# Optimization experiments

Measured on AMD Instinct MI355X. Metric: run time of the kernel, lower is better.

Reference implementation:

```python
import jax, jax.numpy as jnp
import numpy as np

MODEL_DIM = 1024
NUM_HEADS = 16
HEAD_DIM = MODEL_DIM // NUM_HEADS


def setup_inputs() -> dict:
    key = jax.random.key(0)
    ks = jax.random.split(key, 9)
    s = 1.0 / np.sqrt(MODEL_DIM)
    d = {
        "query": jax.random.normal(ks[0], (2, 2048, MODEL_DIM), dtype=jnp.float32),
        "Wq": jax.random.normal(ks[1], (MODEL_DIM, MODEL_DIM), dtype=jnp.float32) * s,
        "bq": jnp.zeros((MODEL_DIM,), dtype=jnp.float32),
        "Wk": jax.random.normal(ks[2], (MODEL_DIM, MODEL_DIM), dtype=jnp.float32) * s,
        "bk": jnp.zeros((MODEL_DIM,), dtype=jnp.float32),
        "Wv": jax.random.normal(ks[3], (MODEL_DIM, MODEL_DIM), dtype=jnp.float32) * s,
        "bv": jnp.zeros((MODEL_DIM,), dtype=jnp.float32),
        "Wo": jax.random.normal(ks[4], (MODEL_DIM, MODEL_DIM), dtype=jnp.float32) * s,
        "bo": jnp.zeros((MODEL_DIM,), dtype=jnp.float32),
    }
    return d


def reference(query, Wq, bq, Wk, bk, Wv, bv, Wo, bo):
    B, S, D = query.shape
    H, hd = NUM_HEADS, HEAD_DIM
    # self-attention: key = value = query
    q = (query @ Wq.T + bq).reshape(B, S, H, hd).transpose(0, 2, 1, 3)  # [B,H,S,hd]
    k = (query @ Wk.T + bk).reshape(B, S, H, hd).transpose(0, 2, 1, 3)
    v = (query @ Wv.T + bv).reshape(B, S, H, hd).transpose(0, 2, 1, 3)
    scores = jnp.einsum("bhqd,bhkd->bhqk", q, k) / np.sqrt(hd)  # [B,H,S,S]
    attn = jax.nn.softmax(scores, axis=-1)
    ctx = jnp.einsum("bhqk,bhkd->bhqd", attn, v)  # [B,H,S,hd]
    ctx = ctx.transpose(0, 2, 1, 3).reshape(B, S, D)
    return ctx @ Wo.T + bo
```

## Files before the change

kernel.cpp:

```cpp
#include <hip/hip_runtime.h>

typedef __attribute__((ext_vector_type(8))) __bf16 bf16x8;
typedef __attribute__((ext_vector_type(8))) unsigned short ushort8;
typedef __attribute__((ext_vector_type(4))) unsigned short ushort4v;
typedef __attribute__((ext_vector_type(4))) float f32x4;
typedef __attribute__((ext_vector_type(2))) _Float16 f16x2;
typedef __attribute__((ext_vector_type(4))) _Float16 f16x4;
typedef __attribute__((ext_vector_type(8))) _Float16 f16x8;
typedef __attribute__((ext_vector_type(2))) __fp16 fp16v2;

__device__ __forceinline__ unsigned short f2bf(float f) {
    union { float f; unsigned int u; } c; c.f = f;
    unsigned int u = c.u;
    u += 0x7fffu + ((u >> 16) & 1u);
    return (unsigned short)(u >> 16);
}

__device__ __forceinline__ void async16(const void* g, void* l) {
    __builtin_amdgcn_global_load_lds(
        (const __attribute__((address_space(1))) unsigned int*)g,
        (__attribute__((address_space(3))) unsigned int*)l, 16, 0, 0);
}

__global__ __launch_bounds__(256) void cvt_all(
    const float* __restrict__ q,  const float* __restrict__ wq,
    const float* __restrict__ wk, const float* __restrict__ wv,
    const float* __restrict__ wo,
    unsigned short* __restrict__ q_bf, unsigned short* __restrict__ wqkv,
    unsigned short* __restrict__ wo_bf, float scale_k)
{
    const int NQ = 4096 * 1024, NW = 1024 * 1024;
    int i = (blockIdx.x * 256 + threadIdx.x) * 4;
    const float* src; unsigned short* dst; float sc = 1.0f; int off;
    if (i < NQ)               { src = q;  dst = q_bf;          off = i; }
    else if (i < NQ + NW)     { src = wq; dst = wqkv;          off = i - NQ; }
    else if (i < NQ + 2 * NW) { src = wk; dst = wqkv + NW;     off = i - NQ - NW; sc = scale_k; }
    else if (i < NQ + 3 * NW) { src = wv; dst = wqkv + 2 * NW; off = i - NQ - 2 * NW; }
    else                      { src = wo; dst = wo_bf;         off = i - NQ - 3 * NW; }
    float4 v = *(const float4*)(src + off);
    ushort4v o;
    o[0] = f2bf(v.x * sc); o[1] = f2bf(v.y * sc);
    o[2] = f2bf(v.z * sc); o[3] = f2bf(v.w * sc);
    *(ushort4v*)(dst + off) = o;
}

__global__ __launch_bounds__(256) void qkv_gemm(
    const unsigned short* __restrict__ A,
    const unsigned short* __restrict__ B,
    unsigned short* __restrict__ qkv,
    _Float16* __restrict__ vtg,
    const float* __restrict__ b0, const float* __restrict__ b1, const float* __restrict__ b2,
    float s1)
{
    __shared__ __align__(16) unsigned short As[128 * 64];
    __shared__ __align__(16) unsigned short Bs[128 * 64];

    const int tid  = threadIdx.x;
    const int lane = tid & 63, wave = tid >> 6;
    const int quad = lane >> 4, l15 = lane & 15;
    const int wm = wave >> 1, wn = wave & 1;
    const int by = blockIdx.y, bx = blockIdx.x;
    const int K = 1024;

    const int srow = lane >> 3;
    const int sp   = lane & 7;
    const int scl  = sp ^ srow;
    const int sw   = l15 & 7;

    f32x4 acc[4][4];
#pragma unroll
    for (int i = 0; i < 4; ++i)
#pragma unroll
        for (int j = 0; j < 4; ++j) acc[i][j] = (f32x4)(0.0f);

    for (int kt = 0; kt < 16; ++kt) {
        __syncthreads();
#pragma unroll
        for (int j = 0; j < 4; ++j) {
            int r0 = wave * 32 + j * 8;
            async16(A + (size_t)(by * 128 + r0 + srow) * K + kt * 64 + scl * 8, &As[r0 * 64]);
            async16(B + (size_t)(bx * 128 + r0 + srow) * K + kt * 64 + scl * 8, &Bs[r0 * 64]);
        }
        __syncthreads();

#pragma unroll
        for (int kh = 0; kh < 2; ++kh) {
            bf16x8 af[4], bfr[4];
#pragma unroll
            for (int mi = 0; mi < 4; ++mi)
                af[mi] = __builtin_bit_cast(bf16x8,
                    *(const ushort8*)&As[(wm * 64 + mi * 16 + l15) * 64 + ((kh * 4 + quad) ^ sw) * 8]);
#pragma unroll
            for (int ni = 0; ni < 4; ++ni)
                bfr[ni] = __builtin_bit_cast(bf16x8,
                    *(const ushort8*)&Bs[(wn * 64 + ni * 16 + l15) * 64 + ((kh * 4 + quad) ^ sw) * 8]);
#pragma unroll
            for (int mi = 0; mi < 4; ++mi)
#pragma unroll
                for (int ni = 0; ni < 4; ++ni)
                    acc[mi][ni] = __builtin_amdgcn_mfma_f32_16x16x32_bf16(af[mi], bfr[ni], acc[mi][ni], 0, 0, 0);
        }
    }

    if (bx < 16) {
#pragma unroll
        for (int ni = 0; ni < 4; ++ni) {
            int n = bx * 128 + wn * 64 + ni * 16 + l15;
            float bias = (n < 1024) ? b0[n] : b1[n - 1024] * s1;
#pragma unroll
            for (int mi = 0; mi < 4; ++mi) {
#pragma unroll
                for (int r = 0; r < 4; ++r) {
                    int m = by * 128 + wm * 64 + mi * 16 + quad * 4 + r;
                    qkv[(size_t)m * 2048 + n] = f2bf(acc[mi][ni][r] + bias);
                }
            }
        }
    } else {
        const int mb = by * 128 + wm * 64;
        const int b  = mb >> 11;
        const int st = (mb & 2047) >> 6;
#pragma unroll
        for (int ni = 0; ni < 4; ++ni) {
            int vf = (bx - 16) * 128 + wn * 64 + ni * 16 + l15;
            int h = vf >> 6, hd = vf & 63;
            float bias = b2[vf];
            _Float16* vrow = vtg + ((size_t)((b * 16 + h) * 64 + hd)) * 2048 + st * 64;
#pragma unroll
            for (int mi = 0; mi < 4; ++mi) {
                int p = ((mi >> 1) * 4 + quad) ^ (l15 & 7);
                f16x4 o;
#pragma unroll
                for (int r = 0; r < 4; ++r) o[r] = (_Float16)(acc[mi][ni][r] + bias);
                *(f16x4*)(vrow + p * 8 + (mi & 1) * 4) = o;
            }
        }
    }
}

__global__ __launch_bounds__(256) void out_gemm(
    const unsigned short* __restrict__ A,
    const unsigned short* __restrict__ B,
    float* __restrict__ Cout,
    const float* __restrict__ bo)
{
    __shared__ __align__(16) unsigned short As[128 * 64];
    __shared__ __align__(16) unsigned short Bs[64 * 64];

    const int tid  = threadIdx.x;
    const int lane = tid & 63, wave = tid >> 6;
    const int quad = lane >> 4, l15 = lane & 15;
    const int wm = wave >> 1, wn = wave & 1;
    const int by = blockIdx.y, bx = blockIdx.x;
    const int K = 1024;

    const int srow = lane >> 3;
    const int sp   = lane & 7;
    const int scl  = sp ^ srow;
    const int sw   = l15 & 7;

    f32x4 acc[4][2];
#pragma unroll
    for (int i = 0; i < 4; ++i)
#pragma unroll
        for (int j = 0; j < 2; ++j) acc[i][j] = (f32x4)(0.0f);

    for (int kt = 0; kt < 16; ++kt) {
        __syncthreads();
#pragma unroll
        for (int j = 0; j < 4; ++j) {
            int r0 = wave * 32 + j * 8;
            async16(A + (size_t)(by * 128 + r0 + srow) * K + kt * 64 + scl * 8, &As[r0 * 64]);
        }
#pragma unroll
        for (int j = 0; j < 2; ++j) {
            int r0 = wave * 16 + j * 8;
            async16(B + (size_t)(bx * 64 + r0 + srow) * K + kt * 64 + scl * 8, &Bs[r0 * 64]);
        }
        __syncthreads();

#pragma unroll
        for (int kh = 0; kh < 2; ++kh) {
            bf16x8 af[4], bfr[2];
#pragma unroll
            for (int mi = 0; mi < 4; ++mi)
                af[mi] = __builtin_bit_cast(bf16x8,
                    *(const ushort8*)&As[(wm * 64 + mi * 16 + l15) * 64 + ((kh * 4 + quad) ^ sw) * 8]);
#pragma unroll
            for (int ni = 0; ni < 2; ++ni)
                bfr[ni] = __builtin_bit_cast(bf16x8,
                    *(const ushort8*)&Bs[(wn * 32 + ni * 16 + l15) * 64 + ((kh * 4 + quad) ^ sw) * 8]);
#pragma unroll
            for (int mi = 0; mi < 4; ++mi)
#pragma unroll
                for (int ni = 0; ni < 2; ++ni)
                    acc[mi][ni] = __builtin_amdgcn_mfma_f32_16x16x32_bf16(af[mi], bfr[ni], acc[mi][ni], 0, 0, 0);
        }
    }

#pragma unroll
    for (int ni = 0; ni < 2; ++ni) {
        int n = bx * 64 + wn * 32 + ni * 16 + l15;
        float bias = bo[n];
#pragma unroll
        for (int mi = 0; mi < 4; ++mi) {
#pragma unroll
            for (int r = 0; r < 4; ++r) {
                int m = by * 128 + wm * 64 + mi * 16 + quad * 4 + r;
                Cout[(size_t)m * 1024 + n] = acc[mi][ni][r] + bias;
            }
        }
    }
}

__global__ __launch_bounds__(256) void attn(const unsigned short* __restrict__ qkv,
                                            const _Float16* __restrict__ vtg,
                                            unsigned short* __restrict__ ctx)
{
    __shared__ __align__(16) unsigned short Ks[4 * 64 * 64];
    __shared__ __align__(16) _Float16 Vt[4 * 64 * 64];

    const int tid  = threadIdx.x;
    const int lane = tid & 63, wave = tid >> 6;
    const int quad = lane >> 4, l15 = lane & 15;
    const int bh = blockIdx.y;
    const int b = bh >> 4, h = bh & 15;
    const int q0 = blockIdx.x * 128;

    const int srow = lane >> 3;
    const int sp   = lane & 7;
    const int scl  = sp ^ srow;
    const int sw   = l15 & 7;

    bf16x8 qf[2][2];
#pragma unroll
    for (int s = 0; s < 2; ++s) {
        int qrow = b * 2048 + q0 + wave * 32 + s * 16 + l15;
#pragma unroll
        for (int kh = 0; kh < 2; ++kh)
            qf[s][kh] = __builtin_bit_cast(bf16x8,
                *(const ushort8*)(qkv + (size_t)qrow * 2048 + h * 64 + kh * 32 + quad * 8));
    }

    f32x4 ot[2][4];
#pragma unroll
    for (int s = 0; s < 2; ++s)
#pragma unroll
        for (int ht = 0; ht < 4; ++ht) ot[s][ht] = (f32x4)(0.0f);
    float l_acc[2] = {0.0f, 0.0f};
    const fp16v2 ones = {(__fp16)1.0f, (__fp16)1.0f};

    for (int KT = 0; KT < 8; ++KT) {
        __syncthreads();
#pragma unroll
        for (int j = 0; j < 4; ++j) {
            int kt = KT * 4 + j;
#pragma unroll
            for (int i = 0; i < 2; ++i) {
                int row = i * 32 + wave * 8 + srow;
                async16(qkv + (size_t)(b * 2048 + kt * 64 + row) * 2048 + 1024 + h * 64 + scl * 8,
                        &Ks[j * 4096 + (i * 32 + wave * 8) * 64]);
                async16(vtg + (size_t)(bh * 64 + row) * 2048 + kt * 64 + sp * 8,
                        (unsigned short*)&Vt[j * 4096 + (i * 32 + wave * 8) * 64]);
            }
        }
        __syncthreads();

#pragma unroll
        for (int j = 0; j < 4; ++j) {
            const unsigned short* KsJ = &Ks[j * 4096];
            const _Float16*       VtJ = &Vt[j * 4096];

            f16x4 pv[2][4];
#pragma unroll
            for (int mt = 0; mt < 4; ++mt) {
                const unsigned short* kb = &KsJ[(mt * 16 + l15) * 64];
                bf16x8 k0 = __builtin_bit_cast(bf16x8, *(const ushort8*)(kb + (quad ^ sw) * 8));
                bf16x8 k1 = __builtin_bit_cast(bf16x8, *(const ushort8*)(kb + ((quad ^ sw) ^ 4) * 8));
#pragma unroll
                for (int s = 0; s < 2; ++s) {
                    f32x4 s4 = (f32x4)(0.0f);
                    s4 = __builtin_amdgcn_mfma_f32_16x16x32_bf16(k0, qf[s][0], s4, 0, 0, 0);
                    s4 = __builtin_amdgcn_mfma_f32_16x16x32_bf16(k1, qf[s][1], s4, 0, 0, 0);
                    float p0 = __builtin_amdgcn_exp2f(s4[0]);
                    float p1 = __builtin_amdgcn_exp2f(s4[1]);
                    float p2 = __builtin_amdgcn_exp2f(s4[2]);
                    float p3 = __builtin_amdgcn_exp2f(s4[3]);
                    fp16v2 lo = __builtin_amdgcn_cvt_pkrtz(p0, p1);
                    fp16v2 hi = __builtin_amdgcn_cvt_pkrtz(p2, p3);
                    l_acc[s] = __builtin_amdgcn_fdot2(lo, ones, l_acc[s], false);
                    l_acc[s] = __builtin_amdgcn_fdot2(hi, ones, l_acc[s], false);
                    f16x2 lo2 = __builtin_bit_cast(f16x2, lo);
                    f16x2 hi2 = __builtin_bit_cast(f16x2, hi);
                    pv[s][mt] = __builtin_shufflevector(lo2, hi2, 0, 1, 2, 3);
                }
            }

#pragma unroll
            for (int ht = 0; ht < 4; ++ht) {
                const _Float16* vb = &VtJ[(ht * 16 + l15) * 64];
#pragma unroll
                for (int g = 0; g < 2; ++g) {
                    f16x8 v8 = *(const f16x8*)(vb + (((g * 4 + quad) ^ sw)) * 8);
#pragma unroll
                    for (int s = 0; s < 2; ++s) {
                        f16x8 p8 = __builtin_shufflevector(pv[s][2 * g], pv[s][2 * g + 1],
                                                           0, 1, 2, 3, 4, 5, 6, 7);
                        ot[s][ht] = __builtin_amdgcn_mfma_f32_16x16x32_f16(v8, p8, ot[s][ht], 0, 0, 0);
                    }
                }
            }
        }
    }

#pragma unroll
    for (int s = 0; s < 2; ++s) {
        float l = l_acc[s];
        l += __shfl_xor(l, 16, 64);
        l += __shfl_xor(l, 32, 64);
        float inv = 1.0f / l;
        int qrow = b * 2048 + q0 + wave * 32 + s * 16 + l15;
#pragma unroll
        for (int ht = 0; ht < 4; ++ht) {
            ushort4v o4;
#pragma unroll
            for (int r = 0; r < 4; ++r) o4[r] = f2bf(ot[s][ht][r] * inv);
            *(ushort4v*)(ctx + (size_t)qrow * 1024 + h * 64 + ht * 16 + quad * 4) = o4;
        }
    }
}

extern "C" void kernel_launch(void* const* d_in, const int* in_sizes, int n_in,
                              void* d_out, int out_size, void* d_ws, size_t ws_size,
                              hipStream_t stream) {
    const float* query = (const float*)d_in[0];
    const float* Wq = (const float*)d_in[1];
    const float* bq = (const float*)d_in[2];
    const float* Wk = (const float*)d_in[3];
    const float* bk = (const float*)d_in[4];
    const float* Wv = (const float*)d_in[5];
    const float* bv = (const float*)d_in[6];
    const float* Wo = (const float*)d_in[7];
    const float* bo = (const float*)d_in[8];

    char* ws = (char*)d_ws;
    unsigned short* q_bf  = (unsigned short*)(ws);
    unsigned short* ctx   = (unsigned short*)(ws);
    unsigned short* wqkv  = (unsigned short*)(ws + 8388608);
    unsigned short* wo_bf = (unsigned short*)(ws + 14680064);
    unsigned short* qkv   = (unsigned short*)(ws + 16777216);
    _Float16*       vtg   = (_Float16*)(ws + 33554432);

    const float SCALE = 0.125f * 1.4426950408889634f;

    cvt_all<<<8192, 256, 0, stream>>>(query, Wq, Wk, Wv, Wo, q_bf, wqkv, wo_bf, SCALE);
    qkv_gemm<<<dim3(24, 32), 256, 0, stream>>>(q_bf, wqkv, qkv, vtg, bq, bk, bv, SCALE);
    attn<<<dim3(16, 32), 256, 0, stream>>>(qkv, vtg, ctx);
    out_gemm<<<dim3(16, 32), 256, 0, stream>>>(ctx, wo_bf, (float*)d_out, bo);
}
```

Before: 196.7 us.

## Fuse fp32-to-fp16 conversion into GEMM tile loads and drop the conversion kernel

Removes the separate cvt_all pass and has the QKV and output GEMMs load fp32 inputs and weights directly. Each tile is converted to fp16 in registers with packed round-toward-zero conversion before being written to shared memory. The GEMMs switch from bf16 to fp16 MFMA, and the context buffer becomes fp16. This eliminates one launch and a full bf16 write and re-read of the activations and weights. In exchange, each GEMM block re-reads fp32 data (twice the bytes) through synchronous register loads instead of async global-to-LDS copies, which may expose memory latency. fp16 range and RTZ rounding also change numerics.

```diff
diff --git a/kernel.cpp b/kernel.cpp
--- a/kernel.cpp
+++ b/kernel.cpp
@@ -22,31 +22,24 @@
         (__attribute__((address_space(3))) unsigned int*)l, 16, 0, 0);
 }
 
-__global__ __launch_bounds__(256) void cvt_all(
-    const float* __restrict__ q,  const float* __restrict__ wq,
-    const float* __restrict__ wk, const float* __restrict__ wv,
-    const float* __restrict__ wo,
-    unsigned short* __restrict__ q_bf, unsigned short* __restrict__ wqkv,
-    unsigned short* __restrict__ wo_bf, float scale_k)
-{
-    const int NQ = 4096 * 1024, NW = 1024 * 1024;
-    int i = (blockIdx.x * 256 + threadIdx.x) * 4;
-    const float* src; unsigned short* dst; float sc = 1.0f; int off;
-    if (i < NQ)               { src = q;  dst = q_bf;          off = i; }
-    else if (i < NQ + NW)     { src = wq; dst = wqkv;          off = i - NQ; }
-    else if (i < NQ + 2 * NW) { src = wk; dst = wqkv + NW;     off = i - NQ - NW; sc = scale_k; }
-    else if (i < NQ + 3 * NW) { src = wv; dst = wqkv + 2 * NW; off = i - NQ - 2 * NW; }
-    else                      { src = wo; dst = wo_bf;         off = i - NQ - 3 * NW; }
-    float4 v = *(const float4*)(src + off);
-    ushort4v o;
-    o[0] = f2bf(v.x * sc); o[1] = f2bf(v.y * sc);
-    o[2] = f2bf(v.z * sc); o[3] = f2bf(v.w * sc);
-    *(ushort4v*)(dst + off) = o;
+__device__ __forceinline__ ushort8 cvt8(float4 a, float4 b, float sc) {
+    fp16v2 c0 = __builtin_amdgcn_cvt_pkrtz(a.x * sc, a.y * sc);
+    fp16v2 c1 = __builtin_amdgcn_cvt_pkrtz(a.z * sc, a.w * sc);
+    fp16v2 c2 = __builtin_amdgcn_cvt_pkrtz(b.x * sc, b.y * sc);
+    fp16v2 c3 = __builtin_amdgcn_cvt_pkrtz(b.z * sc, b.w * sc);
+    f16x2 d0 = __builtin_bit_cast(f16x2, c0);
+    f16x2 d1 = __builtin_bit_cast(f16x2, c1);
+    f16x2 d2 = __builtin_bit_cast(f16x2, c2);
+    f16x2 d3 = __builtin_bit_cast(f16x2, c3);
+    f16x4 lo = __builtin_shufflevector(d0, d1, 0, 1, 2, 3);
+    f16x4 hi = __builtin_shufflevector(d2, d3, 0, 1, 2, 3);
+    f16x8 v  = __builtin_shufflevector(lo, hi, 0, 1, 2, 3, 4, 5, 6, 7);
+    return __builtin_bit_cast(ushort8, v);
 }
 
 __global__ __launch_bounds__(256) void qkv_gemm(
-    const unsigned short* __restrict__ A,
-    const unsigned short* __restrict__ B,
+    const float* __restrict__ Afp,
+    const float* __restrict__ wq, const float* __restrict__ wk, const float* __restrict__ wv,
     unsigned short* __restrict__ qkv,
     _Float16* __restrict__ vtg,
     const float* __restrict__ b0, const float* __restrict__ b1, const float* __restrict__ b2,
@@ -60,13 +53,17 @@
     const int quad = lane >> 4, l15 = lane & 15;
     const int wm = wave >> 1, wn = wave & 1;
     const int by = blockIdx.y, bx = blockIdx.x;
-    const int K = 1024;
 
     const int srow = lane >> 3;
     const int sp   = lane & 7;
     const int scl  = sp ^ srow;
     const int sw   = l15 & 7;
 
+    const float* wsrc; float bsc;
+    if (bx < 8)       { wsrc = wq + (size_t)bx * 128 * 1024;        bsc = 1.0f; }
+    else if (bx < 16) { wsrc = wk + (size_t)(bx - 8) * 128 * 1024;  bsc = s1;   }
+    else              { wsrc = wv + (size_t)(bx - 16) * 128 * 1024; bsc = 1.0f; }
+
     f32x4 acc[4][4];
 #pragma unroll
     for (int i = 0; i < 4; ++i)
@@ -75,30 +72,54 @@
 
     for (int kt = 0; kt < 16; ++kt) {
         __syncthreads();
-#pragma unroll
-        for (int j = 0; j < 4; ++j) {
-            int r0 = wave * 32 + j * 8;
-            async16(A + (size_t)(by * 128 + r0 + srow) * K + kt * 64 + scl * 8, &As[r0 * 64]);
-            async16(B + (size_t)(bx * 128 + r0 + srow) * K + kt * 64 + scl * 8, &Bs[r0 * 64]);
+        {
+            float4 a0[4], a1[4];
+#pragma unroll
+            for (int j = 0; j < 4; ++j) {
+                int r0 = wave * 32 + j * 8;
+                const float* src = Afp + (size_t)(by * 128 + r0 + srow) * 1024 + kt * 64 + scl * 8;
+                a0[j] = *(const float4*)src;
+                a1[j] = *(const float4*)(src + 4);
+            }
+#pragma unroll
+            for (int j = 0; j < 4; ++j) {
+                int r0 = wave * 32 + j * 8;
+                *(ushort8*)&As[(r0 + srow) * 64 + sp * 8] = cvt8(a0[j], a1[j], 1.0f);
+            }
+        }
+        {
+            float4 w0[4], w1[4];
+#pragma unroll
+            for (int j = 0; j < 4; ++j) {
+                int r0 = wave * 32 + j * 8;
+                const float* src = wsrc + (size_t)(r0 + srow) * 1024 + kt * 64 + scl * 8;
+                w0[j] = *(const float4*)src;
+                w1[j] = *(const float4*)(src + 4);
+            }
+#pragma unroll
+            for (int j = 0; j < 4; ++j) {
+                int r0 = wave * 32 + j * 8;
+                *(ushort8*)&Bs[(r0 + srow) * 64 + sp * 8] = cvt8(w0[j], w1[j], bsc);
+            }
         }
         __syncthreads();
 
 #pragma unroll
         for (int kh = 0; kh < 2; ++kh) {
-            bf16x8 af[4], bfr[4];
+            f16x8 af[4], bfr[4];
 #pragma unroll
             for (int mi = 0; mi < 4; ++mi)
-                af[mi] = __builtin_bit_cast(bf16x8,
+                af[mi] = __builtin_bit_cast(f16x8,
                     *(const ushort8*)&As[(wm * 64 + mi * 16 + l15) * 64 + ((kh * 4 + quad) ^ sw) * 8]);
 #pragma unroll
             for (int ni = 0; ni < 4; ++ni)
-                bfr[ni] = __builtin_bit_cast(bf16x8,
+                bfr[ni] = __builtin_bit_cast(f16x8,
                     *(const ushort8*)&Bs[(wn * 64 + ni * 16 + l15) * 64 + ((kh * 4 + quad) ^ sw) * 8]);
 #pragma unroll
             for (int mi = 0; mi < 4; ++mi)
 #pragma unroll
                 for (int ni = 0; ni < 4; ++ni)
-                    acc[mi][ni] = __builtin_amdgcn_mfma_f32_16x16x32_bf16(af[mi], bfr[ni], acc[mi][ni], 0, 0, 0);
+                    acc[mi][ni] = __builtin_amdgcn_mfma_f32_16x16x32_f16(af[mi], bfr[ni], acc[mi][ni], 0, 0, 0);
         }
     }
 
@@ -139,8 +160,8 @@
 }
 
 __global__ __launch_bounds__(256) void out_gemm(
-    const unsigned short* __restrict__ A,
-    const unsigned short* __restrict__ B,
+    const _Float16* __restrict__ A,
+    const float* __restrict__ B,
     float* __restrict__ Cout,
     const float* __restrict__ bo)
 {
@@ -152,7 +173,6 @@
     const int quad = lane >> 4, l15 = lane & 15;
     const int wm = wave >> 1, wn = wave & 1;
     const int by = blockIdx.y, bx = blockIdx.x;
-    const int K = 1024;
 
     const int srow = lane >> 3;
     const int sp   = lane & 7;
@@ -170,31 +190,41 @@
 #pragma unroll
         for (int j = 0; j < 4; ++j) {
             int r0 = wave * 32 + j * 8;
-            async16(A + (size_t)(by * 128 + r0 + srow) * K + kt * 64 + scl * 8, &As[r0 * 64]);
-        }
-#pragma unroll
-        for (int j = 0; j < 2; ++j) {
-            int r0 = wave * 16 + j * 8;
-            async16(B + (size_t)(bx * 64 + r0 + srow) * K + kt * 64 + scl * 8, &Bs[r0 * 64]);
+            async16(A + (size_t)(by * 128 + r0 + srow) * 1024 + kt * 64 + scl * 8, &As[r0 * 64]);
+        }
+        {
+            float4 w0[2], w1[2];
+#pragma unroll
+            for (int j = 0; j < 2; ++j) {
+                int r0 = wave * 16 + j * 8;
+                const float* src = B + (size_t)(bx * 64 + r0 + srow) * 1024 + kt * 64 + scl * 8;
+                w0[j] = *(const float4*)src;
+                w1[j] = *(const float4*)(src + 4);
+            }
+#pragma unroll
+            for (int j = 0; j < 2; ++j) {
+                int r0 = wave * 16 + j * 8;
+                *(ushort8*)&Bs[(r0 + srow) * 64 + sp * 8] = cvt8(w0[j], w1[j], 1.0f);
+            }
         }
         __syncthreads();
 
 #pragma unroll
         for (int kh = 0; kh < 2; ++kh) {
-            bf16x8 af[4], bfr[2];
+            f16x8 af[4], bfr[2];
 #pragma unroll
             for (int mi = 0; mi < 4; ++mi)
-                af[mi] = __builtin_bit_cast(bf16x8,
+                af[mi] = __builtin_bit_cast(f16x8,
                     *(const ushort8*)&As[(wm * 64 + mi * 16 + l15) * 64 + ((kh * 4 + quad) ^ sw) * 8]);
 #pragma unroll
             for (int ni = 0; ni < 2; ++ni)
-                bfr[ni] = __builtin_bit_cast(bf16x8,
+                bfr[ni] = __builtin_bit_cast(f16x8,
                     *(const ushort8*)&Bs[(wn * 32 + ni * 16 + l15) * 64 + ((kh * 4 + quad) ^ sw) * 8]);
 #pragma unroll
             for (int mi = 0; mi < 4; ++mi)
 #pragma unroll
                 for (int ni = 0; ni < 2; ++ni)
-                    acc[mi][ni] = __builtin_amdgcn_mfma_f32_16x16x32_bf16(af[mi], bfr[ni], acc[mi][ni], 0, 0, 0);
+                    acc[mi][ni] = __builtin_amdgcn_mfma_f32_16x16x32_f16(af[mi], bfr[ni], acc[mi][ni], 0, 0, 0);
         }
     }
 
@@ -215,7 +245,7 @@
 
 __global__ __launch_bounds__(256) void attn(const unsigned short* __restrict__ qkv,
                                             const _Float16* __restrict__ vtg,
-                                            unsigned short* __restrict__ ctx)
+                                            _Float16* __restrict__ ctx)
 {
     __shared__ __align__(16) unsigned short Ks[4 * 64 * 64];
     __shared__ __align__(16) _Float16 Vt[4 * 64 * 64];
@@ -322,10 +352,10 @@
         int qrow = b * 2048 + q0 + wave * 32 + s * 16 + l15;
 #pragma unroll
         for (int ht = 0; ht < 4; ++ht) {
-            ushort4v o4;
-#pragma unroll
-            for (int r = 0; r < 4; ++r) o4[r] = f2bf(ot[s][ht][r] * inv);
-            *(ushort4v*)(ctx + (size_t)qrow * 1024 + h * 64 + ht * 16 + quad * 4) = o4;
+            f16x4 o4;
+#pragma unroll
+            for (int r = 0; r < 4; ++r) o4[r] = (_Float16)(ot[s][ht][r] * inv);
+            *(f16x4*)(ctx + (size_t)qrow * 1024 + h * 64 + ht * 16 + quad * 4) = o4;
         }
     }
 }
@@ -344,17 +374,13 @@
     const float* bo = (const float*)d_in[8];
 
     char* ws = (char*)d_ws;
-    unsigned short* q_bf  = (unsigned short*)(ws);
-    unsigned short* ctx   = (unsigned short*)(ws);
-    unsigned short* wqkv  = (unsigned short*)(ws + 8388608);
-    unsigned short* wo_bf = (unsigned short*)(ws + 14680064);
+    _Float16*       ctx   = (_Float16*)(ws);
     unsigned short* qkv   = (unsigned short*)(ws + 16777216);
     _Float16*       vtg   = (_Float16*)(ws + 33554432);
 
     const float SCALE = 0.125f * 1.4426950408889634f;
 
-    cvt_all<<<8192, 256, 0, stream>>>(query, Wq, Wk, Wv, Wo, q_bf, wqkv, wo_bf, SCALE);
-    qkv_gemm<<<dim3(24, 32), 256, 0, stream>>>(q_bf, wqkv, qkv, vtg, bq, bk, bv, SCALE);
+    qkv_gemm<<<dim3(24, 32), 256, 0, stream>>>(query, Wq, Wk, Wv, qkv, vtg, bq, bk, bv, SCALE);
     attn<<<dim3(16, 32), 256, 0, stream>>>(qkv, vtg, ctx);
-    out_gemm<<<dim3(16, 32), 256, 0, stream>>>(ctx, wo_bf, (float*)d_out, bo);
-}
+    out_gemm<<<dim3(16, 32), 256, 0, stream>>>(ctx, Wo, (float*)d_out, bo);
+}
```

Measured after the change: 202.7 us. +3.0%, slower.
